# Optimization experiments

Hardware: AMD Instinct MI355X
Metric: run time of the kernel (lower is better)

Reference implementation:

```python
import jax, jax.numpy as jnp
import numpy as np

N, E, ESM, H, OUT, L, NG = 20000, 640000, 1280, 128, 256, 3, 64
NV, EV = 4, 1  # node/edge vector channels
MSG_S, MSG_V = 2 * H + H, 2 * NV + EV   # 384, 9
UPD_S, UPD_V = 2 * H, 2 * NV            # 256, 8


def _safe_norm(v):
    # exact ||v|| with zero (not nan) gradient at v == 0
    n2 = jnp.sum(v * v, axis=-1)
    pos = n2 > 0
    return jnp.sqrt(jnp.where(pos, n2, 1.0)) * pos


def _normalize(x, eps=1e-12):
    n = _safe_norm(x)[..., None]
    return jnp.where(n > 0, x / jnp.maximum(n, eps), 0.0)


def _ln(x, g, b, eps=1e-5):
    m = x.mean(-1, keepdims=True)
    v = ((x - m) ** 2).mean(-1, keepdims=True)
    return (x - m) / jnp.sqrt(v + eps) * g + b


def _gvp(s, v, Wss, Wvs, Wsv, Wvv, g, b):
    # s: [M, Cs], v: [M, Cv, 3]
    vn = _safe_norm(v)                                        # [M, Cv]
    s_out = jax.nn.gelu(_ln(s @ Wss.T + vn @ Wvs.T, g, b), approximate=False)
    v_out = jnp.einsum('mic,oi->moc', v, Wvv)                 # [M, Cvo, 3]
    v_out = v_out * jax.nn.sigmoid(s @ Wsv.T)[:, :, None]     # gate from input s
    return s_out, v_out


def _compute_node_vectors(coords, cb):
    ca_cb = _normalize(cb - coords)
    ca_next = jnp.roll(coords, -1, axis=0)
    d = (ca_next - coords).at[-1].set(0.0)
    d = _normalize(d)
    normal = _normalize(jnp.cross(ca_cb, d))
    t = (ca_next - jnp.roll(coords, 1, axis=0)).at[0].set(0.0).at[-1].set(0.0)
    t = _normalize(t)
    return jnp.stack([ca_cb, d, normal, t], axis=1)           # [N, 4, 3]


def setup_inputs() -> dict:
    key = jax.random.key(0)
    ks = jax.random.split(key, 32)

    def w(k, shape):
        return (jax.random.normal(k, shape, jnp.float32) / np.sqrt(shape[-1])).astype(jnp.float32)

    inp = {
        'esm_features': jax.random.normal(ks[0], (N, ESM), jnp.float32),
        'geometric_features': jax.random.normal(ks[1], (N, 15), jnp.float32),
        'node_coords': jax.random.normal(ks[2], (N, 3), jnp.float32) * 10.0,
        'edge_index': jax.random.randint(ks[3], (2, E), 0, N, jnp.int32),
        'edge_attr': jax.random.normal(ks[4], (E, 16), jnp.float32),
        'batch_index': jnp.sort(jax.random.randint(ks[5], (N,), 0, NG, jnp.int32)),
        # projections
        'node_proj_W': w(ks[6], (H, ESM + 9)), 'node_proj_b': jnp.zeros((H,), jnp.float32),
        'edge_proj_W': w(ks[7], (H, 13)), 'edge_proj_b': jnp.zeros((H,), jnp.float32),
        # message GVP (stacked over L layers)
        'msg_Wss': w(ks[8], (L, H, MSG_S)), 'msg_Wvs': w(ks[9], (L, H, MSG_V)),
        'msg_Wsv': w(ks[10], (L, NV, MSG_S)), 'msg_Wvv': w(ks[11], (L, NV, MSG_V)),
        'msg_ln_g': jnp.ones((L, H), jnp.float32), 'msg_ln_b': jnp.zeros((L, H), jnp.float32),
        # update GVP
        'upd_Wss': w(ks[12], (L, H, UPD_S)), 'upd_Wvs': w(ks[13], (L, H, UPD_V)),
        'upd_Wsv': w(ks[14], (L, NV, UPD_S)), 'upd_Wvv': w(ks[15], (L, NV, UPD_V)),
        'upd_ln_g': jnp.ones((L, H), jnp.float32), 'upd_ln_b': jnp.zeros((L, H), jnp.float32),
        # heads
        'node_out_W': w(ks[16], (ESM, H)), 'node_out_b': jnp.zeros((ESM,), jnp.float32),
        'graph_out_W': w(ks[17], (OUT, H)), 'graph_out_b': jnp.zeros((OUT,), jnp.float32),
    }
    return inp


def reference(esm_features, geometric_features, node_coords, edge_index, edge_attr,
              batch_index, node_proj_W, node_proj_b, edge_proj_W, edge_proj_b,
              msg_Wss, msg_Wvs, msg_Wsv, msg_Wvv, msg_ln_g, msg_ln_b,
              upd_Wss, upd_Wvs, upd_Wsv, upd_Wvv, upd_ln_g, upd_ln_b,
              node_out_W, node_out_b, graph_out_W, graph_out_b):
    n = esm_features.shape[0]
    cb = geometric_features[:, 3:6]
    geo_scalar = geometric_features[:, 6:15]
    node_s = jnp.concatenate([esm_features, geo_scalar], -1) @ node_proj_W.T + node_proj_b
    node_v = _compute_node_vectors(node_coords, cb)
    edge_s = jnp.concatenate([edge_attr[:, 0:2], edge_attr[:, 5:]], -1) @ edge_proj_W.T + edge_proj_b
    edge_v = edge_attr[:, 2:5][:, None, :]                    # [E, 1, 3]
    src, dst = edge_index[0], edge_index[1]
    for l in range(msg_Wss.shape[0]):
        ms = jnp.concatenate([node_s[src], node_s[dst], edge_s], -1)   # [E, 3H]
        mv = jnp.concatenate([node_v[src], node_v[dst], edge_v], 1)    # [E, 9, 3]
        ms, mv = _gvp(ms, mv, msg_Wss[l], msg_Wvs[l], msg_Wsv[l], msg_Wvv[l],
                      msg_ln_g[l], msg_ln_b[l])
        ag_s = jnp.zeros((n, ms.shape[1]), ms.dtype).at[dst].add(ms)
        ag_v = jnp.zeros((n, mv.shape[1], 3), mv.dtype).at[dst].add(mv)
        us = jnp.concatenate([node_s, ag_s], -1)
        uv = jnp.concatenate([node_v, ag_v], 1)
        ns, nv = _gvp(us, uv, upd_Wss[l], upd_Wvs[l], upd_Wsv[l], upd_Wvv[l],
                      upd_ln_g[l], upd_ln_b[l])
        node_s = node_s + ns
        node_v = node_v + nv
    updated_nodes = node_s @ node_out_W.T + node_out_b
    gfeat = node_s @ graph_out_W.T + graph_out_b
    cnt = jax.ops.segment_sum(jnp.ones((n,), gfeat.dtype), batch_index, NG)
    graph_emb = jax.ops.segment_sum(gfeat, batch_index, NG) / jnp.maximum(cnt, 1.0)[:, None]
    return graph_emb, updated_nodes
```

## Files before the change

### kernel.cpp

```cpp
#include <hip/hip_runtime.h>
#include <math.h>

#define DEVI __device__ __forceinline__

namespace {

constexpr int NN = 20000;
constexpr int NE = 640000;

typedef __attribute__((ext_vector_type(8))) short s8v;
typedef __attribute__((ext_vector_type(4))) float f4v;

DEVI float gelu_f(float x){ return 0.5f*x*(1.0f+erff(x*0.70710678118654752440f)); }
DEVI float gelu_t(float x){
  float u = x*x;
  float z = x*(1.59576912f + 0.07135481f*u);
  return x / (1.f + __expf(-z));
}
DEVI float sigm(float x){ return 1.0f/(1.0f+expf(-x)); }
DEVI float sigm_f(float x){ return 1.0f/(1.0f+__expf(-x)); }
DEVI unsigned bf_rne(float f){ unsigned u=__float_as_uint(f); return (u + 0x7fffu + ((u>>16)&1u)) >> 16; }

struct F3{ float x,y,z; };
DEVI F3 sub3(F3 a, F3 b){ return F3{a.x-b.x, a.y-b.y, a.z-b.z}; }
DEVI F3 cross3(F3 a, F3 b){ return F3{a.y*b.z-a.z*b.y, a.z*b.x-a.x*b.z, a.x*b.y-a.y*b.x}; }
DEVI F3 snorm3(F3 v){
  float n2 = v.x*v.x+v.y*v.y+v.z*v.z;
  if(n2 > 0.f){ float inv = 1.0f/sqrtf(n2); return F3{v.x*inv, v.y*inv, v.z*inv}; }
  return F3{0.f,0.f,0.f};
}

__global__ void k_prep(const float* __restrict__ npW, const float* __restrict__ noW,
                       const float* __restrict__ goW,
                       const float* __restrict__ mWss, const float* __restrict__ mWvs,
                       const float* __restrict__ uWss, const float* __restrict__ uWvs,
                       unsigned short* __restrict__ npW_bf, float* __restrict__ Wt_no,
                       float* __restrict__ Wt_go,
                       float* __restrict__ Wt_mss, float* __restrict__ Wt_mvs,
                       float* __restrict__ Wt_uss, float* __restrict__ Wt_uvs){
  int b = blockIdx.x, t = threadIdx.x;
  if(b >= 1563){
    int idx = (b-1563)*256 + t;
    if(idx < 128*1408){
      int r = idx/1408, c = idx-r*1408;
      npW_bf[idx] = (c<1289) ? (unsigned short)bf_rne(npW[(size_t)r*1289+c]) : (unsigned short)0;
    }
    return;
  }
  const float* src; float* dst; int R,C,ld,base,elems;
  if(b<640){ src=noW; dst=Wt_no; R=1280;C=128;ld=128; base=0; elems=163840; }
  else if(b<768){ src=goW; dst=Wt_go; R=256;C=128;ld=128; base=640; elems=32768; }
  else {
    int bb=b-768; int l=bb/265; int r=bb-l*265;
    if(r<128){ src=mWss+(size_t)l*128*384; dst=Wt_mss+(size_t)l*256*128; R=128;C=256;ld=384; base=768+l*265; elems=32768; }
    else if(r<133){ src=mWvs+(size_t)l*128*9; dst=Wt_mvs+(size_t)l*9*128; R=128;C=9;ld=9; base=768+l*265+128; elems=1152; }
    else if(r<261){ src=uWss+(size_t)l*128*256; dst=Wt_uss+(size_t)l*256*128; R=128;C=256;ld=256; base=768+l*265+133; elems=32768; }
    else { src=uWvs+(size_t)l*128*8; dst=Wt_uvs+(size_t)l*8*128; R=128;C=8;ld=8; base=768+l*265+261; elems=1024; }
  }
  int idx=(b-base)*256+t;
  if(idx>=elems) return;
  int r=idx/C, c=idx%C;
  dst[c*R+r] = src[r*ld+c];
}

__global__ void k_conv(const float* __restrict__ esm, const float* __restrict__ geo,
                       unsigned short* __restrict__ esm_bf){
  int idx = blockIdx.x*256 + threadIdx.x;
  if(idx >= 20000*176) return;
  int r = idx/176, c = idx - r*176;
  int k = c*8;
  float v0,v1,v2,v3,v4,v5,v6,v7;
  if(k+8 <= 1280){
    const float4* p = reinterpret_cast<const float4*>(esm + (size_t)r*1280 + k);
    float4 x=p[0], y=p[1];
    v0=x.x;v1=x.y;v2=x.z;v3=x.w;v4=y.x;v5=y.y;v6=y.z;v7=y.w;
  } else {
    float vv[8];
#pragma unroll
    for(int j=0;j<8;j++){
      int kk=k+j;
      vv[j] = (kk<1280)? esm[(size_t)r*1280+kk] : ((kk<1289)? geo[r*15+6+(kk-1280)] : 0.f);
    }
    v0=vv[0];v1=vv[1];v2=vv[2];v3=vv[3];v4=vv[4];v5=vv[5];v6=vv[6];v7=vv[7];
  }
  uint4 w;
  w.x = bf_rne(v0) | (bf_rne(v1)<<16);
  w.y = bf_rne(v2) | (bf_rne(v3)<<16);
  w.z = bf_rne(v4) | (bf_rne(v5)<<16);
  w.w = bf_rne(v6) | (bf_rne(v7)<<16);
  reinterpret_cast<uint4*>(esm_bf)[idx] = w;
}

__global__ __launch_bounds__(256,4) void k_init(
    const unsigned short* __restrict__ esm_bf, const unsigned short* __restrict__ npW_bf,
    float* __restrict__ part){
  int t = threadIdx.x;
  int b = blockIdx.x;
  int ks = b & 3, nb = b >> 2;
  int wv = t>>6, lane = t&63;
  int row0 = nb*64 + wv*16;
  int arow = row0 + (lane&15);
  int arc = (arow < NN) ? arow : (NN-1);
  int kb = (lane>>4)*8;
  const unsigned short* ap = esm_bf + (size_t)arc*1408 + ks*352 + kb;
  const unsigned short* bp = npW_bf + (size_t)(lane&15)*1408 + ks*352 + kb;
// ... 15 lines not shown
    int o = nt*16+col;
#pragma unroll
    for(int r=0;r<4;r++){
      int row = row0 + r4 + r;
      if(row<NN) po[(size_t)row*128+o] = acc[nt][r];
    }
  }
}

__global__ void k_reduce(const float* __restrict__ part, const float* __restrict__ bias,
                         float* __restrict__ node_s){
  int idx = blockIdx.x*256 + threadIdx.x;
  int o = idx & 127;
  node_s[idx] = bias[o] + part[idx] + part[(size_t)NN*128+idx]
              + part[2*(size_t)NN*128+idx] + part[3*(size_t)NN*128+idx];
}

__global__ void k_nodevec(const float* __restrict__ coords, const float* __restrict__ geo,
                          float* __restrict__ node_v,
                          int* __restrict__ counts, int* __restrict__ cntg){
  int n = blockIdx.x*256 + threadIdx.x;
  if(n<64) cntg[n]=0;
  if(n>=NN) return;
  counts[n]=0;
  F3 c  {coords[n*3], coords[n*3+1], coords[n*3+2]};
  F3 cb {geo[n*15+3], geo[n*15+4], geo[n*15+5]};
  F3 cacb = snorm3(sub3(cb, c));
  F3 d{0.f,0.f,0.f};
  if(n < NN-1){
    F3 nx {coords[(n+1)*3], coords[(n+1)*3+1], coords[(n+1)*3+2]};
    d = snorm3(sub3(nx, c));
  }
  F3 nor = snorm3(cross3(cacb, d));
  F3 tv{0.f,0.f,0.f};
  if(n>0 && n<NN-1){
    F3 nx {coords[(n+1)*3], coords[(n+1)*3+1], coords[(n+1)*3+2]};
    F3 pv {coords[(n-1)*3], coords[(n-1)*3+1], coords[(n-1)*3+2]};
    tv = snorm3(sub3(nx, pv));
  }
  float* p = node_v + n*12;
  p[0]=cacb.x; p[1]=cacb.y; p[2]=cacb.z;
  p[3]=d.x;    p[4]=d.y;    p[5]=d.z;
  p[6]=nor.x;  p[7]=nor.y;  p[8]=nor.z;
  p[9]=tv.x;   p[10]=tv.y;  p[11]=tv.z;
}

__global__ void k_hist(const int* __restrict__ eidx, const int* __restrict__ batch,
                       int* __restrict__ counts, int* __restrict__ cntg){
  int i = blockIdx.x*256+threadIdx.x;
  if(i<NE) atomicAdd(&counts[eidx[NE+i]], 1);
  if(i<NN) atomicAdd(&cntg[batch[i]], 1);
}
__global__ void k_scan1(const int* __restrict__ counts, int* __restrict__ bsums){
  __shared__ int red[256];
  int b=blockIdx.x, t=threadIdx.x;
  int base=b*512;
  int v=0;
  for(int i=t;i<512;i+=256){ int g=base+i; if(g<NN) v+=counts[g]; }
  red[t]=v; __syncthreads();
// ... 88 lines not shown
#pragma unroll
    for(int n=0;n<16;n++){
      float4 s4 = *reinterpret_cast<const float4*>(&s_l[n][k]);
      acc[n] = fmaf(s4.x,w0,acc[n]); acc[n] = fmaf(s4.y,w1,acc[n]);
      acc[n] = fmaf(s4.z,w2,acc[n]); acc[n] = fmaf(s4.w,w3,acc[n]);
    }
  }
  const float* Wv = Wt_vs + h*4*128;
#pragma unroll
  for(int j=0;j<4;j++){
    float w = Wv[j*128+o];
#pragma unroll
    for(int n=0;n<16;n++) acc[n] += nv_l[n][j]*w;
  }
  float* P = h ? P_b : P_a;
#pragma unroll
  for(int n=0;n<16;n++) P[(size_t)(n0+n)*128+o] = acc[n];
}

__global__ void k_econst3(const float* __restrict__ mWss, const float* __restrict__ mWvs,
                          const float* __restrict__ mWsv, const float* __restrict__ mWvv,
                          const float* __restrict__ Wep, const float* __restrict__ epb,
                          float* __restrict__ econ){
  int l = blockIdx.x;
  const float* Wss = mWss + (size_t)l*128*384;
  const float* Wvs = mWvs + (size_t)l*128*9;
  const float* Wsv = mWsv + (size_t)l*4*384;
  const float* Wvv = mWvv + (size_t)l*4*9;
  float* ec = econ + (size_t)l*2048;
  int t=threadIdx.x;
  for(int idx=t; idx<13*128; idx+=256){
    int j=idx>>7, o=idx&127;
    float s=0.f;
    for(int k=0;k<128;k++) s += Wss[o*384+256+k]*Wep[k*13+j];
    ec[j*128+o]=s;
  }
  for(int o=t;o<128;o+=256){
    float s=0.f;
    for(int k=0;k<128;k++) s += Wss[o*384+256+k]*epb[k];
    ec[1664+o]=s;
    ec[1792+o]=Wvs[o*9+8];
  }
  if(t<52){ int c=t/13,j=t%13; float s=0.f; for(int k=0;k<128;k++) s+=Wsv[c*384+256+k]*Wep[k*13+j]; ec[1920+t]=s; }
  if(t<4){ float s=0.f; for(int k=0;k<128;k++) s+=Wsv[t*384+256+k]*epb[k]; ec[1972+t]=s; ec[1976+t]=Wvv[t*9+8]; }
}

__global__ __launch_bounds__(256,4) void k_edge(
    const float* __restrict__ ea_s, const float* __restrict__ ec,
    unsigned* __restrict__ preS2, float* __restrict__ preG){
  int t = threadIdx.x;
  int lane = t&63;
  int wid = blockIdx.x*4 + (t>>6);
  float mex[13], mey[13];
#pragma unroll
  for(int j=0;j<13;j++){ mex[j]=ec[j*128+lane]; mey[j]=ec[j*128+64+lane]; }
  float bx=ec[1664+lane], by=ec[1664+64+lane];
  float w8x=ec[1792+lane], w8y=ec[1792+64+lane];
  int cg = (lane<4)?lane:0;
  float grc[13];
// ... 34 lines not shown
      g=fmaf(grc[3],e3,g);  g=fmaf(grc[4],e4,g);  g=fmaf(grc[5],e5,g);
      g=fmaf(grc[6],e6,g);  g=fmaf(grc[7],e7,g);  g=fmaf(grc[8],e8,g);
      g=fmaf(grc[9],e9,g);  g=fmaf(grc[10],e10,g); g=fmaf(grc[11],e11,g);
      g=fmaf(grc[12],e12,g);
      preG[(size_t)e*8+lane] = g;
    } else if(lane<7){
      float evv = (lane==4)?evx:((lane==5)?evy:evz);
      preG[(size_t)e*8+lane] = evv;
    }
  }
}

#define DECLST(P) unsigned P##w=0; float P##pax=0.f,P##pay=0.f,P##g8=0.f,P##ev=0.f,P##ga=0.f,P##va=0.f;
#define LOADST(P, IDX) do{ int _p=(IDX); int _s=srcp[_p]; \
  P##w   = preS2[_p*64 + lane]; \
  P##pax = P_a[_s*128+lane]; P##pay = P_a[_s*128+64+lane]; \
  if(lane<12){ P##g8 = preG[_p*8+cv]; P##ev = preG[_p*8+4+xv]; \
               P##ga = G_a[_s*4+cv];  P##va = V_a[_s*12+lane]; } \
}while(0)
#define COMPUTE(P) do{ \
  float px = __uint_as_float(P##w<<16); \
  float py = __uint_as_float(P##w & 0xffff0000u); \
  float pre0 = px + P##pax + PBx; \
  float pre1 = py + P##pay + PBy; \
  float sm = pre0+pre1; \
  float sq = pre0*pre0 + pre1*pre1; \
  _Pragma("unroll") \
  for(int m=32;m;m>>=1){ sm += __shfl_xor(sm,m); sq += __shfl_xor(sq,m); } \
  float mean = sm*0.0078125f; \
  float var  = fmaf(sq,0.0078125f, -mean*mean); \
  float rstd = rsqrtf((var>0.f?var:0.f) + 1e-5f); \
// ... 6 lines not shown
  } \
}while(0)

__global__ __launch_bounds__(256,8) void k_msg(
                      const float* __restrict__ P_a, const float* __restrict__ P_b,
                      const float* __restrict__ G_a, const float* __restrict__ G_b,
                      const float* __restrict__ V_a, const float* __restrict__ V_b,
                      const unsigned* __restrict__ preS2, const float* __restrict__ preG,
                      const int* __restrict__ srcp, const int* __restrict__ offs,
                      const float* __restrict__ ec,
                      const float* __restrict__ lng, const float* __restrict__ lnb,
                      float* __restrict__ ag_s, float* __restrict__ ag_v){
  int t = threadIdx.x;
  int n = blockIdx.x*4 + (t>>6);
  int lane = t&63;
  float PBx = P_b[n*128+lane], PBy = P_b[n*128+64+lane];
  float LGx = lng[lane], LGy = lng[64+lane];
  float LBx = lnb[lane], LBy = lnb[64+lane];
  int cv = lane/3, xv = lane - cv*3;
  float vbk=0.f, gbn=0.f, wvc=0.f;
  if(lane<12){
    vbk = V_b[n*12+lane];
    gbn = G_b[n*4+cv];
    wvc = ec[1976+cv];
  }
  float accx=0.f, accy=0.f, avk=0.f;
  int beg = offs[n], end = offs[n+1];
  DECLST(a_) DECLST(b_)
  int idx = beg;
  if(beg < end) LOADST(a_, beg);
  while(idx + 1 < end){
    LOADST(b_, idx+1);
    COMPUTE(a_);
    if(idx + 2 < end) LOADST(a_, idx+2);
    COMPUTE(b_);
    idx += 2;
  }
  if(idx < end) COMPUTE(a_);
  ag_s[n*128+lane]    = accx;
  ag_s[n*128+64+lane] = accy;
  if(lane<12) ag_v[n*12+lane] = avk;
}

__global__ __launch_bounds__(256,4) void k_update(
                         float* __restrict__ node_s, float* __restrict__ node_v,
                         const float* __restrict__ ag_s, const float* __restrict__ ag_v,
                         const float* __restrict__ Wt_ss, const float* __restrict__ Wt_vs,
                         const float* __restrict__ Wsv, const float* __restrict__ Wvv,
                         const float* __restrict__ lng, const float* __restrict__ lnb){
  __shared__ float us[16][260];
  __shared__ float pre[16][129];
  __shared__ float uv[16][24];
  __shared__ float uvn[16][8];
  __shared__ float stats[16][2];
  __shared__ float gate_l[16][4];
  int t = threadIdx.x;
  int n0 = blockIdx.x*16;
  for(int idx=t; idx<2048; idx+=256){
    int n = idx>>7, k = idx&127;
    us[n][k]     = node_s[(size_t)(n0+n)*128+k];
    us[n][128+k] = ag_s[(size_t)(n0+n)*128+k];
  }
  for(int idx=t; idx<384; idx+=256){
    int n = idx/24, k = idx%24;
    uv[n][k] = (k<12) ? node_v[(n0+n)*12+k] : ag_v[(n0+n)*12 + (k-12)];
  }
  __syncthreads();
  if(t<128){
    int n=t>>3, j=t&7;
    float x=uv[n][j*3], y=uv[n][j*3+1], z=uv[n][j*3+2];
    float n2=x*x+y*y+z*z;
    uvn[n][j] = n2>0.f ? sqrtf(n2) : 0.f;
  }
  __syncthreads();
  int o = t&127, h = t>>7;
  float acc[8];
#pragma unroll
  for(int i=0;i<8;i++) acc[i]=0.f;
  for(int k=0;k<256;k+=4){
    float w0=Wt_ss[(k+0)*128+o], w1=Wt_ss[(k+1)*128+o], w2=Wt_ss[(k+2)*128+o], w3=Wt_ss[(k+3)*128+o];
#pragma unroll
    for(int i=0;i<8;i++){
      float4 s4 = *reinterpret_cast<const float4*>(&us[h*8+i][k]);
      acc[i] = fmaf(s4.x,w0,acc[i]); acc[i] = fmaf(s4.y,w1,acc[i]);
      acc[i] = fmaf(s4.z,w2,acc[i]); acc[i] = fmaf(s4.w,w3,acc[i]);
    }
  }
#pragma unroll
  for(int j=0;j<8;j++){
    float w = Wt_vs[j*128+o];
#pragma unroll
    for(int i=0;i<8;i++) acc[i] += uvn[h*8+i][j]*w;
  }
#pragma unroll
  for(int i=0;i<8;i++) pre[h*8+i][o] = acc[i];
  __syncthreads();
  {
    int n = t>>4, p = t&15;
    float s=0.f;
#pragma unroll
    for(int q=0;q<8;q++) s += pre[n][p*8+q];
#pragma unroll
    for(int m=8;m;m>>=1) s += __shfl_xor(s,m);
    float mean = s*(1.f/128.f);
    float v=0.f;
#pragma unroll
    for(int q=0;q<8;q++){ float d=pre[n][p*8+q]-mean; v += d*d; }
#pragma unroll
    for(int m=8;m;m>>=1) v += __shfl_xor(v,m);
    if(p==0){ stats[n][0]=mean; stats[n][1]=rsqrtf(v*(1.f/128.f)+1e-5f); }
  }
  __syncthreads();
  {
    float LG = lng[o], LB = lnb[o];
#pragma unroll
    for(int i=0;i<8;i++){
      int n = h*8+i;
      float hh = (pre[n][o]-stats[n][0])*stats[n][1]*LG + LB;
      node_s[(size_t)(n0+n)*128+o] += gelu_f(hh);
    }
  }
  {
    int n = t>>4, c = t&3, p = (t>>2)&3;
    float g=0.f;
    int kb = p*64;
    for(int k=0;k<64;k+=4){
      float4 s4 = *reinterpret_cast<const float4*>(&us[n][kb+k]);
      g = fmaf(s4.x,Wsv[c*256+kb+k],g);   g = fmaf(s4.y,Wsv[c*256+kb+k+1],g);
      g = fmaf(s4.z,Wsv[c*256+kb+k+2],g); g = fmaf(s4.w,Wsv[c*256+kb+k+3],g);
    }
    g += __shfl_xor(g,4);
    g += __shfl_xor(g,8);
    if(p==0) gate_l[n][c] = sigm(g);
  }
  __syncthreads();
  if(t<192){
    int n = t/12, k = t%12, c = k/3, x = k-c*3;
    float s=0.f;
#pragma unroll
    for(int j=0;j<8;j++) s += Wvv[c*8+j]*uv[n][j*3+x];
    node_v[(n0+n)*12+k] += s*gate_l[n][c];
  }
}

__global__ __launch_bounds__(256,8) void k_out(
    const float* __restrict__ node_s, const float* __restrict__ Wt_no,
    const float* __restrict__ nob, float* __restrict__ out){
  __shared__ float s_l[32][132];
  int t = threadIdx.x;
  int n0 = blockIdx.x*32;
  int oc0 = blockIdx.y*256;
  {
    const float4* g = reinterpret_cast<const float4*>(node_s + (size_t)n0*128);
    for(int i=t;i<1024;i+=256){
      int n=i>>5, kq=i&31;
      *reinterpret_cast<float4*>(&s_l[n][kq*4]) = g[i];
    }
  }
  __syncthreads();
  int oq = t&63, ng = t>>6;
  int o = oc0 + oq*4;
  float4 acc[8];
#pragma unroll
  for(int i=0;i<8;i++) acc[i]=float4{0.f,0.f,0.f,0.f};
  for(int k=0;k<128;k+=4){
    float4 w0 = *reinterpret_cast<const float4*>(&Wt_no[(k+0)*1280+o]);
    float4 w1 = *reinterpret_cast<const float4*>(&Wt_no[(k+1)*1280+o]);
    float4 w2 = *reinterpret_cast<const float4*>(&Wt_no[(k+2)*1280+o]);
    float4 w3 = *reinterpret_cast<const float4*>(&Wt_no[(k+3)*1280+o]);
#pragma unroll
    for(int i=0;i<8;i++){
      float4 s = *reinterpret_cast<const float4*>(&s_l[ng*8+i][k]);
      acc[i].x=fmaf(s.x,w0.x,acc[i].x); acc[i].y=fmaf(s.x,w0.y,acc[i].y);
      acc[i].z=fmaf(s.x,w0.z,acc[i].z); acc[i].w=fmaf(s.x,w0.w,acc[i].w);
      acc[i].x=fmaf(s.y,w1.x,acc[i].x); acc[i].y=fmaf(s.y,w1.y,acc[i].y);
      acc[i].z=fmaf(s.y,w1.z,acc[i].z); acc[i].w=fmaf(s.y,w1.w,acc[i].w);
      acc[i].x=fmaf(s.z,w2.x,acc[i].x); acc[i].y=fmaf(s.z,w2.y,acc[i].y);
      acc[i].z=fmaf(s.z,w2.z,acc[i].z); acc[i].w=fmaf(s.z,w2.w,acc[i].w);
      acc[i].x=fmaf(s.w,w3.x,acc[i].x); acc[i].y=fmaf(s.w,w3.y,acc[i].y);
      acc[i].z=fmaf(s.w,w3.z,acc[i].z); acc[i].w=fmaf(s.w,w3.w,acc[i].w);
    }
  }
  float4 b4 = *reinterpret_cast<const float4*>(&nob[o]);
#pragma unroll
  for(int i=0;i<8;i++){
    int row = n0 + ng*8 + i;
    float4 r{acc[i].x+b4.x, acc[i].y+b4.y, acc[i].z+b4.z, acc[i].w+b4.w};
    *reinterpret_cast<float4*>(&out[16384 + (size_t)row*1280 + o]) = r;
  }
}

__global__ __launch_bounds__(256,4) void k_gfeat(
                        const float* __restrict__ node_s, const float* __restrict__ Wt,
                        const int* __restrict__ batch, float* __restrict__ gacc){
  __shared__ float s_l[16][128];
  __shared__ int b_l[16];
  int t=threadIdx.x, n0=blockIdx.x*16;
  for(int idx=t; idx<2048; idx+=256){ int n=idx>>7,k=idx&127; s_l[n][k]=node_s[(size_t)(n0+n)*128+k]; }
  if(t<16) b_l[t]=batch[n0+t];
  __syncthreads();
  int o=t;
  float acc[16];
#pragma unroll
  for(int i=0;i<16;i++) acc[i]=0.f;
  for(int k=0;k<128;k+=4){
    float w0=Wt[(k+0)*256+o], w1=Wt[(k+1)*256+o], w2=Wt[(k+2)*256+o], w3=Wt[(k+3)*256+o];
#pragma unroll
    for(int n=0;n<16;n++){
      float4 s4 = *reinterpret_cast<const float4*>(&s_l[n][k]);
      acc[n] = fmaf(s4.x,w0,acc[n]); acc[n] = fmaf(s4.y,w1,acc[n]);
      acc[n] = fmaf(s4.z,w2,acc[n]); acc[n] = fmaf(s4.w,w3,acc[n]);
    }
  }
  float run=0.f; int cur=b_l[0];
#pragma unroll
  for(int n=0;n<16;n++){
    int g=b_l[n];
    if(g!=cur){ atomicAdd(&gacc[cur*256+o], run); run=0.f; cur=g; }
    run += acc[n];
  }
  atomicAdd(&gacc[cur*256+o], run);
}

__global__ void k_gfin(const float* __restrict__ gacc, const int* __restrict__ cntg,
                       const float* __restrict__ gob, float* __restrict__ out){
  int g=blockIdx.x, o=threadIdx.x;
  int c=cntg[g];
  out[g*256+o] = (c>0) ? (gacc[g*256+o]/(float)c + gob[o]) : 0.f;
}

}

extern "C" void kernel_launch(void* const* d_in, const int* in_sizes, int n_in,
                              void* d_out, int out_size, void* d_ws, size_t ws_size,
                              hipStream_t stream){
  (void)in_sizes; (void)n_in; (void)out_size;
// ... 54 lines not shown
  float* gacc   = (float*)ALLOC((size_t)64*256*4);
  int* counts = (int*)ALLOC((size_t)NN*4);
  int* offs   = (int*)ALLOC((size_t)(NN+1)*4);
  int* cursor = (int*)ALLOC((size_t)NN*4);
  int* bsums  = (int*)ALLOC((size_t)64*4);
  int* cntg   = (int*)ALLOC((size_t)64*4);
  int* srcp   = (int*)ALLOC((size_t)NE*4);
  float* ea_s = (float*)ALLOC((size_t)NE*16*4);
  unsigned* preS2 = (unsigned*)ALLOC((size_t)NE*64*4);
  float* preG     = (float*)ALLOC((size_t)NE*8*4);
  if(off > ws_size) return;
  float* part = (float*)preS2;

  hipMemsetAsync(gacc, 0, (size_t)64*256*4, stream);

  k_prep<<<2267,256,0,stream>>>(npW, noW, goW, mWss, mWvs, uWss, uWvs,
                                npW_bf, Wt_no, Wt_go, Wt_mss, Wt_mvs, Wt_uss, Wt_uvs);
  k_conv<<<13750,256,0,stream>>>(esm, geo, esm_bf);
  k_init<<<1252,256,0,stream>>>(esm_bf, npW_bf, part);
  k_reduce<<<10000,256,0,stream>>>(part, npb, node_s);
  k_nodevec<<<79,256,0,stream>>>(coords, geo, node_v, counts, cntg);
  k_hist<<<2500,256,0,stream>>>(eidx, batch, counts, cntg);
  k_scan1<<<40,256,0,stream>>>(counts, bsums);
  k_scan23<<<40,256,0,stream>>>(counts, bsums, offs, cursor);
  k_fill<<<2500,256,0,stream>>>(eidx, cursor, eattr, srcp, ea_s);
  k_econst3<<<3,256,0,stream>>>(mWss, mWvs, mWsv, mWvv, epW, epb, econ);

  for(int l=0;l<3;l++){
    k_pre<<<1250,256,0,stream>>>(node_s, node_v,
                                 Wt_mss + (size_t)l*256*128, Wt_mvs + (size_t)l*9*128,
                                 mWsv + (size_t)l*4*384, mWvv + (size_t)l*4*9,
                                 P_a, P_b, G_a, G_b, V_a, V_b);
    k_edge<<<20000,256,0,stream>>>(ea_s, econ + (size_t)l*2048, preS2, preG);
    k_msg<<<5000,256,0,stream>>>(P_a, P_b, G_a, G_b, V_a, V_b, preS2, preG, srcp, offs,
                                 econ + (size_t)l*2048, mlg + (size_t)l*128, mlb + (size_t)l*128,
                                 ag_s, ag_v);
    k_update<<<1250,256,0,stream>>>(node_s, node_v, ag_s, ag_v,
                                    Wt_uss + (size_t)l*256*128, Wt_uvs + (size_t)l*8*128,
                                    uWsv + (size_t)l*4*256, uWvv + (size_t)l*4*8,
                                    ulg + (size_t)l*128, ulb + (size_t)l*128);
  }
  k_out<<<dim3(625,5),256,0,stream>>>(node_s, Wt_no, nob, out);
  k_gfeat<<<1250,256,0,stream>>>(node_s, Wt_go, batch, gacc);
  k_gfin<<<64,256,0,stream>>>(gacc, cntg, gob, out);
}
```

Measured before the change: 1.549 ms.

## Fuse prep kernels, fold next-layer pre into update, merge output kernels

Merges the weight-transpose, bf16 conversion, node-vector and edge-constant kernels into one large k_prep launch. The next layer's message precompute (P/G/V projections) is folded into the update kernel, so updated node features are reused from shared memory instead of being reloaded. The output and graph-feature GEMMs are combined into one launch. P_a/P_b are stored interleaved so k_msg can read them with float2 loads. This cuts launch count and global round-trips, at the cost of a longer update kernel with more barriers and shared-memory state.

New measurement: 1.572 ms. No clear change (+1.5%).

```diff
diff --git a/kernel.cpp b/kernel.cpp
--- a/kernel.cpp
+++ b/kernel.cpp
@@ -33,13 +33,36 @@
 __global__ void k_prep(const float* __restrict__ npW, const float* __restrict__ noW,
                        const float* __restrict__ goW,
                        const float* __restrict__ mWss, const float* __restrict__ mWvs,
+                       const float* __restrict__ mWsv, const float* __restrict__ mWvv,
                        const float* __restrict__ uWss, const float* __restrict__ uWvs,
-                       unsigned short* __restrict__ npW_bf, float* __restrict__ Wt_no,
-                       float* __restrict__ Wt_go,
+                       const float* __restrict__ Wep, const float* __restrict__ epb,
+                       const float* __restrict__ esm, const float* __restrict__ geo,
+                       const float* __restrict__ coords,
+                       unsigned short* __restrict__ npW_bf, unsigned short* __restrict__ esm_bf,
+                       float* __restrict__ Wt_no, float* __restrict__ Wt_go,
                        float* __restrict__ Wt_mss, float* __restrict__ Wt_mvs,
-                       float* __restrict__ Wt_uss, float* __restrict__ Wt_uvs){
+                       float* __restrict__ Wt_uss, float* __restrict__ Wt_uvs,
+                       float* __restrict__ econ, float* __restrict__ node_v,
+                       int* __restrict__ counts, int* __restrict__ cntg){
   int b = blockIdx.x, t = threadIdx.x;
-  if(b >= 1563){
+  if(b < 1563){
+    const float* src; float* dst; int R,C,ld,base,elems;
+    if(b<640){ src=noW; dst=Wt_no; R=1280;C=128;ld=128; base=0; elems=163840; }
+    else if(b<768){ src=goW; dst=Wt_go; R=256;C=128;ld=128; base=640; elems=32768; }
+    else {
+      int bb=b-768; int l=bb/265; int r=bb-l*265;
+      if(r<128){ src=mWss+(size_t)l*128*384; dst=Wt_mss+(size_t)l*256*128; R=128;C=256;ld=384; base=768+l*265; elems=32768; }
+      else if(r<133){ src=mWvs+(size_t)l*128*9; dst=Wt_mvs+(size_t)l*9*128; R=128;C=9;ld=9; base=768+l*265+128; elems=1152; }
+      else if(r<261){ src=uWss+(size_t)l*128*256; dst=Wt_uss+(size_t)l*256*128; R=128;C=256;ld=256; base=768+l*265+133; elems=32768; }
+      else { src=uWvs+(size_t)l*128*8; dst=Wt_uvs+(size_t)l*8*128; R=128;C=8;ld=8; base=768+l*265+261; elems=1024; }
+    }
+    int idx=(b-base)*256+t;
+    if(idx>=elems) return;
+    int r=idx/C, c=idx%C;
+    dst[c*R+r] = src[r*ld+c];
+    return;
+  }
+  if(b < 2267){
     int idx = (b-1563)*256 + t;
     if(idx < 128*1408){
       int r = idx/1408, c = idx-r*1408;
@@ -47,48 +70,82 @@
     }
     return;
   }
-  const float* src; float* dst; int R,C,ld,base,elems;
-  if(b<640){ src=noW; dst=Wt_no; R=1280;C=128;ld=128; base=0; elems=163840; }
-  else if(b<768){ src=goW; dst=Wt_go; R=256;C=128;ld=128; base=640; elems=32768; }
-  else {
-    int bb=b-768; int l=bb/265; int r=bb-l*265;
-    if(r<128){ src=mWss+(size_t)l*128*384; dst=Wt_mss+(size_t)l*256*128; R=128;C=256;ld=384; base=768+l*265; elems=32768; }
-    else if(r<133){ src=mWvs+(size_t)l*128*9; dst=Wt_mvs+(size_t)l*9*128; R=128;C=9;ld=9; base=768+l*265+128; elems=1152; }
-    else if(r<261){ src=uWss+(size_t)l*128*256; dst=Wt_uss+(size_t)l*256*128; R=128;C=256;ld=256; base=768+l*265+133; elems=32768; }
-    else { src=uWvs+(size_t)l*128*8; dst=Wt_uvs+(size_t)l*8*128; R=128;C=8;ld=8; base=768+l*265+261; elems=1024; }
-  }
-  int idx=(b-base)*256+t;
-  if(idx>=elems) return;
-  int r=idx/C, c=idx%C;
-  dst[c*R+r] = src[r*ld+c];
-}
-
-__global__ void k_conv(const float* __restrict__ esm, const float* __restrict__ geo,
-                       unsigned short* __restrict__ esm_bf){
-  int idx = blockIdx.x*256 + threadIdx.x;
-  if(idx >= 20000*176) return;
-  int r = idx/176, c = idx - r*176;
-  int k = c*8;
-  float v0,v1,v2,v3,v4,v5,v6,v7;
-  if(k+8 <= 1280){
-    const float4* p = reinterpret_cast<const float4*>(esm + (size_t)r*1280 + k);
-    float4 x=p[0], y=p[1];
-    v0=x.x;v1=x.y;v2=x.z;v3=x.w;v4=y.x;v5=y.y;v6=y.z;v7=y.w;
-  } else {
-    float vv[8];
-#pragma unroll
-    for(int j=0;j<8;j++){
-      int kk=k+j;
-      vv[j] = (kk<1280)? esm[(size_t)r*1280+kk] : ((kk<1289)? geo[r*15+6+(kk-1280)] : 0.f);
-    }
-    v0=vv[0];v1=vv[1];v2=vv[2];v3=vv[3];v4=vv[4];v5=vv[5];v6=vv[6];v7=vv[7];
-  }
-  uint4 w;
-  w.x = bf_rne(v0) | (bf_rne(v1)<<16);
-  w.y = bf_rne(v2) | (bf_rne(v3)<<16);
-  w.z = bf_rne(v4) | (bf_rne(v5)<<16);
-  w.w = bf_rne(v6) | (bf_rne(v7)<<16);
-  reinterpret_cast<uint4*>(esm_bf)[idx] = w;
+  if(b < 16017){
+    int idx = (b-2267)*256 + t;
+    if(idx >= 20000*176) return;
+    int r = idx/176, c = idx - r*176;
+    int k = c*8;
+    float v0,v1,v2,v3,v4,v5,v6,v7;
+    if(k+8 <= 1280){
+      const float4* p = reinterpret_cast<const float4*>(esm + (size_t)r*1280 + k);
+      float4 x=p[0], y=p[1];
+      v0=x.x;v1=x.y;v2=x.z;v3=x.w;v4=y.x;v5=y.y;v6=y.z;v7=y.w;
+    } else {
+      float vv[8];
+#pragma unroll
+      for(int j=0;j<8;j++){
+        int kk=k+j;
+        vv[j] = (kk<1280)? esm[(size_t)r*1280+kk] : ((kk<1289)? geo[r*15+6+(kk-1280)] : 0.f);
+      }
+      v0=vv[0];v1=vv[1];v2=vv[2];v3=vv[3];v4=vv[4];v5=vv[5];v6=vv[6];v7=vv[7];
+    }
+    uint4 w;
+    w.x = bf_rne(v0) | (bf_rne(v1)<<16);
+    w.y = bf_rne(v2) | (bf_rne(v3)<<16);
+    w.z = bf_rne(v4) | (bf_rne(v5)<<16);
+    w.w = bf_rne(v6) | (bf_rne(v7)<<16);
+    reinterpret_cast<uint4*>(esm_bf)[idx] = w;
+    return;
+  }
+  if(b < 16096){
+    int n = (b-16017)*256 + t;
+    if(n<64) cntg[n]=0;
+    if(n>=NN) return;
+    counts[n]=0;
+    F3 c  {coords[n*3], coords[n*3+1], coords[n*3+2]};
+    F3 cb {geo[n*15+3], geo[n*15+4], geo[n*15+5]};
+    F3 cacb = snorm3(sub3(cb, c));
+    F3 d{0.f,0.f,0.f};
+    if(n < NN-1){
+      F3 nx {coords[(n+1)*3], coords[(n+1)*3+1], coords[(n+1)*3+2]};
+      d = snorm3(sub3(nx, c));
+    }
+    F3 nor = snorm3(cross3(cacb, d));
+    F3 tv{0.f,0.f,0.f};
+    if(n>0 && n<NN-1){
+      F3 nx {coords[(n+1)*3], coords[(n+1)*3+1], coords[(n+1)*3+2]};
+      F3 pv {coords[(n-1)*3], coords[(n-1)*3+1], coords[(n-1)*3+2]};
+      tv = snorm3(sub3(nx, pv));
+    }
+    float* p = node_v + n*12;
+    p[0]=cacb.x; p[1]=cacb.y; p[2]=cacb.z;
+    p[3]=d.x;    p[4]=d.y;    p[5]=d.z;
+    p[6]=nor.x;  p[7]=nor.y;  p[8]=nor.z;
+    p[9]=tv.x;   p[10]=tv.y;  p[11]=tv.z;
+    return;
+  }
+  {
+    int l = b - 16096;
+    const float* Wss = mWss + (size_t)l*128*384;
+    const float* Wvs = mWvs + (size_t)l*128*9;
+    const float* Wsv = mWsv + (size_t)l*4*384;
+    const float* Wvv = mWvv + (size_t)l*4*9;
+    float* ec = econ + (size_t)l*2048;
+    for(int idx=t; idx<13*128; idx+=256){
+      int j=idx>>7, o=idx&127;
+      float s=0.f;
+      for(int k=0;k<128;k++) s += Wss[o*384+256+k]*Wep[k*13+j];
+      ec[j*128+o]=s;
+    }
+    for(int o=t;o<128;o+=256){
+      float s=0.f;
+      for(int k=0;k<128;k++) s += Wss[o*384+256+k]*epb[k];
+      ec[1664+o]=s;
+      ec[1792+o]=Wvs[o*9+8];
+    }
+    if(t<52){ int c=t/13,j=t%13; float s=0.f; for(int k=0;k<128;k++) s+=Wsv[c*384+256+k]*Wep[k*13+j]; ec[1920+t]=s; }
+    if(t<4){ float s=0.f; for(int k=0;k<128;k++) s+=Wsv[t*384+256+k]*epb[k]; ec[1972+t]=s; ec[1976+t]=Wvv[t*9+8]; }
+  }
 }
 
 __global__ __launch_bounds__(256,4) void k_init(
@@ -134,35 +191,6 @@
   int o = idx & 127;
   node_s[idx] = bias[o] + part[idx] + part[(size_t)NN*128+idx]
               + part[2*(size_t)NN*128+idx] + part[3*(size_t)NN*128+idx];
-}
-
-__global__ void k_nodevec(const float* __restrict__ coords, const float* __restrict__ geo,
-                          float* __restrict__ node_v,
-                          int* __restrict__ counts, int* __restrict__ cntg){
-  int n = blockIdx.x*256 + threadIdx.x;
-  if(n<64) cntg[n]=0;
-  if(n>=NN) return;
-  counts[n]=0;
-  F3 c  {coords[n*3], coords[n*3+1], coords[n*3+2]};
-  F3 cb {geo[n*15+3], geo[n*15+4], geo[n*15+5]};
-  F3 cacb = snorm3(sub3(cb, c));
-  F3 d{0.f,0.f,0.f};
-  if(n < NN-1){
-    F3 nx {coords[(n+1)*3], coords[(n+1)*3+1], coords[(n+1)*3+2]};
-    d = snorm3(sub3(nx, c));
-  }
-  F3 nor = snorm3(cross3(cacb, d));
-  F3 tv{0.f,0.f,0.f};
-  if(n>0 && n<NN-1){
-    F3 nx {coords[(n+1)*3], coords[(n+1)*3+1], coords[(n+1)*3+2]};
-    F3 pv {coords[(n-1)*3], coords[(n-1)*3+1], coords[(n-1)*3+2]};
-    tv = snorm3(sub3(nx, pv));
-  }
-  float* p = node_v + n*12;
-  p[0]=cacb.x; p[1]=cacb.y; p[2]=cacb.z;
-  p[3]=d.x;    p[4]=d.y;    p[5]=d.z;
-  p[6]=nor.x;  p[7]=nor.y;  p[8]=nor.z;
-  p[9]=tv.x;   p[10]=tv.y;  p[11]=tv.z;
 }
 
 __global__ void k_hist(const int* __restrict__ eidx, const int* __restrict__ batch,
@@ -281,35 +309,9 @@
     for(int n=0;n<16;n++) acc[n] += nv_l[n][j]*w;
   }
   float* P = h ? P_b : P_a;
-#pragma unroll
-  for(int n=0;n<16;n++) P[(size_t)(n0+n)*128+o] = acc[n];
-}
-
-__global__ void k_econst3(const float* __restrict__ mWss, const float* __restrict__ mWvs,
-                          const float* __restrict__ mWsv, const float* __restrict__ mWvv,
-                          const float* __restrict__ Wep, const float* __restrict__ epb,
-                          float* __restrict__ econ){
-  int l = blockIdx.x;
-  const float* Wss = mWss + (size_t)l*128*384;
-  const float* Wvs = mWvs + (size_t)l*128*9;
-  const float* Wsv = mWsv + (size_t)l*4*384;
-  const float* Wvv = mWvv + (size_t)l*4*9;
-  float* ec = econ + (size_t)l*2048;
-  int t=threadIdx.x;
-  for(int idx=t; idx<13*128; idx+=256){
-    int j=idx>>7, o=idx&127;
-    float s=0.f;
-    for(int k=0;k<128;k++) s += Wss[o*384+256+k]*Wep[k*13+j];
-    ec[j*128+o]=s;
-  }
-  for(int o=t;o<128;o+=256){
-    float s=0.f;
-    for(int k=0;k<128;k++) s += Wss[o*384+256+k]*epb[k];
-    ec[1664+o]=s;
-    ec[1792+o]=Wvs[o*9+8];
-  }
-  if(t<52){ int c=t/13,j=t%13; float s=0.f; for(int k=0;k<128;k++) s+=Wsv[c*384+256+k]*Wep[k*13+j]; ec[1920+t]=s; }
-  if(t<4){ float s=0.f; for(int k=0;k<128;k++) s+=Wsv[t*384+256+k]*epb[k]; ec[1972+t]=s; ec[1976+t]=Wvv[t*9+8]; }
+  int oo = ((o&63)<<1) | (o>>6);
+#pragma unroll
+  for(int n=0;n<16;n++) P[(size_t)(n0+n)*128+oo] = acc[n];
 }
 
 __global__ __launch_bounds__(256,4) void k_edge(
@@ -374,7 +376,8 @@
 #define DECLST(P) unsigned P##w=0; float P##pax=0.f,P##pay=0.f,P##g8=0.f,P##ev=0.f,P##ga=0.f,P##va=0.f;
 #define LOADST(P, IDX) do{ int _p=(IDX); int _s=srcp[_p]; \
   P##w   = preS2[_p*64 + lane]; \
-  P##pax = P_a[_s*128+lane]; P##pay = P_a[_s*128+64+lane]; \
+  float2 _pa = *reinterpret_cast<const float2*>(P_a + _s*128 + 2*lane); \
+  P##pax = _pa.x; P##pay = _pa.y; \
   if(lane<12){ P##g8 = preG[_p*8+cv]; P##ev = preG[_p*8+4+xv]; \
                P##ga = G_a[_s*4+cv];  P##va = V_a[_s*12+lane]; } \
 }while(0)
@@ -411,7 +414,8 @@
   int t = threadIdx.x;
   int n = blockIdx.x*4 + (t>>6);
   int lane = t&63;
-  float PBx = P_b[n*128+lane], PBy = P_b[n*128+64+lane];
+  float2 pb2 = *reinterpret_cast<const float2*>(P_b + n*128 + 2*lane);
+  float PBx = pb2.x, PBy = pb2.y;
   float LGx = lng[lane], LGy = lng[64+lane];
   float LBx = lnb[lane], LBy = lnb[64+lane];
   int cv = lane/3, xv = lane - cv*3;
@@ -439,18 +443,25 @@
   if(lane<12) ag_v[n*12+lane] = avk;
 }
 
-__global__ __launch_bounds__(256,4) void k_update(
+__global__ __launch_bounds__(256,4) void k_updpre(
                          float* __restrict__ node_s, float* __restrict__ node_v,
                          const float* __restrict__ ag_s, const float* __restrict__ ag_v,
                          const float* __restrict__ Wt_ss, const float* __restrict__ Wt_vs,
                          const float* __restrict__ Wsv, const float* __restrict__ Wvv,
-                         const float* __restrict__ lng, const float* __restrict__ lnb){
+                         const float* __restrict__ lng, const float* __restrict__ lnb,
+                         int has_pre,
+                         const float* __restrict__ nWt_ss, const float* __restrict__ nWt_vs,
+                         const float* __restrict__ nWsv, const float* __restrict__ nWvv,
+                         float* __restrict__ P_a, float* __restrict__ P_b,
+                         float* __restrict__ G_a, float* __restrict__ G_b,
+                         float* __restrict__ V_a, float* __restrict__ V_b){
   __shared__ float us[16][260];
   __shared__ float pre[16][129];
   __shared__ float uv[16][24];
   __shared__ float uvn[16][8];
   __shared__ float stats[16][2];
   __shared__ float gate_l[16][4];
+  __shared__ float nvp[16][4];
   int t = threadIdx.x;
   int n0 = blockIdx.x*16;
   for(int idx=t; idx<2048; idx+=256){
@@ -468,54 +479,6 @@
     float x=uv[n][j*3], y=uv[n][j*3+1], z=uv[n][j*3+2];
     float n2=x*x+y*y+z*z;
     uvn[n][j] = n2>0.f ? sqrtf(n2) : 0.f;
-  }
-  __syncthreads();
-  int o = t&127, h = t>>7;
-  float acc[8];
-#pragma unroll
-  for(int i=0;i<8;i++) acc[i]=0.f;
-  for(int k=0;k<256;k+=4){
-    float w0=Wt_ss[(k+0)*128+o], w1=Wt_ss[(k+1)*128+o], w2=Wt_ss[(k+2)*128+o], w3=Wt_ss[(k+3)*128+o];
-#pragma unroll
-    for(int i=0;i<8;i++){
-      float4 s4 = *reinterpret_cast<const float4*>(&us[h*8+i][k]);
-      acc[i] = fmaf(s4.x,w0,acc[i]); acc[i] = fmaf(s4.y,w1,acc[i]);
-      acc[i] = fmaf(s4.z,w2,acc[i]); acc[i] = fmaf(s4.w,w3,acc[i]);
-    }
-  }
-#pragma unroll
-  for(int j=0;j<8;j++){
-    float w = Wt_vs[j*128+o];
-#pragma unroll
-    for(int i=0;i<8;i++) acc[i] += uvn[h*8+i][j]*w;
-  }
-#pragma unroll
-  for(int i=0;i<8;i++) pre[h*8+i][o] = acc[i];
-  __syncthreads();
-  {
-    int n = t>>4, p = t&15;
-    float s=0.f;
-#pragma unroll
-    for(int q=0;q<8;q++) s += pre[n][p*8+q];
-#pragma unroll
-    for(int m=8;m;m>>=1) s += __shfl_xor(s,m);
-    float mean = s*(1.f/128.f);
-    float v=0.f;
-#pragma unroll
-    for(int q=0;q<8;q++){ float d=pre[n][p*8+q]-mean; v += d*d; }
-#pragma unroll
-    for(int m=8;m;m>>=1) v += __shfl_xor(v,m);
-    if(p==0){ stats[n][0]=mean; stats[n][1]=rsqrtf(v*(1.f/128.f)+1e-5f); }
-  }
-  __syncthreads();
-  {
-    float LG = lng[o], LB = lnb[o];
-#pragma unroll
-    for(int i=0;i<8;i++){
-      int n = h*8+i;
-      float hh = (pre[n][o]-stats[n][0])*stats[n][1]*LG + LB;
-      node_s[(size_t)(n0+n)*128+o] += gelu_f(hh);
-    }
   }
   {
     int n = t>>4, c = t&3, p = (t>>2)&3;
@@ -531,92 +494,211 @@
     if(p==0) gate_l[n][c] = sigm(g);
   }
   __syncthreads();
+  int o = t&127, h = t>>7;
+  {
+    float acc[8];
+#pragma unroll
+    for(int i=0;i<8;i++) acc[i]=0.f;
+    for(int k=0;k<256;k+=4){
+      float w0=Wt_ss[(k+0)*128+o], w1=Wt_ss[(k+1)*128+o], w2=Wt_ss[(k+2)*128+o], w3=Wt_ss[(k+3)*128+o];
+#pragma unroll
+      for(int i=0;i<8;i++){
+        float4 s4 = *reinterpret_cast<const float4*>(&us[h*8+i][k]);
+        acc[i] = fmaf(s4.x,w0,acc[i]); acc[i] = fmaf(s4.y,w1,acc[i]);
+        acc[i] = fmaf(s4.z,w2,acc[i]); acc[i] = fmaf(s4.w,w3,acc[i]);
+      }
+    }
+#pragma unroll
+    for(int j=0;j<8;j++){
+      float w = Wt_vs[j*128+o];
+#pragma unroll
+      for(int i=0;i<8;i++) acc[i] += uvn[h*8+i][j]*w;
+    }
+#pragma unroll
+    for(int i=0;i<8;i++) pre[h*8+i][o] = acc[i];
+  }
+  __syncthreads();
+  {
+    int n = t>>4, p = t&15;
+    float s=0.f;
+#pragma unroll
+    for(int q=0;q<8;q++) s += pre[n][p*8+q];
+#pragma unroll
+    for(int m=8;m;m>>=1) s += __shfl_xor(s,m);
+    float mean = s*(1.f/128.f);
+    float v=0.f;
+#pragma unroll
+    for(int q=0;q<8;q++){ float d=pre[n][p*8+q]-mean; v += d*d; }
+#pragma unroll
+    for(int m=8;m;m>>=1) v += __shfl_xor(v,m);
+    if(p==0){ stats[n][0]=mean; stats[n][1]=rsqrtf(v*(1.f/128.f)+1e-5f); }
+  }
+  __syncthreads();
+  {
+    float LG = lng[o], LB = lnb[o];
+#pragma unroll
+    for(int i=0;i<8;i++){
+      int n = h*8+i;
+      float hh = (pre[n][o]-stats[n][0])*stats[n][1]*LG + LB;
+      float val = us[n][o] + gelu_f(hh);
+      node_s[(size_t)(n0+n)*128+o] = val;
+      us[n][o] = val;
+    }
+  }
+  float nvv = 0.f; int vn=0, vk=0;
   if(t<192){
-    int n = t/12, k = t%12, c = k/3, x = k-c*3;
+    vn = t/12; vk = t%12;
+    int c = vk/3, x = vk-c*3;
     float s=0.f;
 #pragma unroll
-    for(int j=0;j<8;j++) s += Wvv[c*8+j]*uv[n][j*3+x];
-    node_v[(n0+n)*12+k] += s*gate_l[n][c];
-  }
-}
-
-__global__ __launch_bounds__(256,8) void k_out(
+    for(int j=0;j<8;j++) s += Wvv[c*8+j]*uv[vn][j*3+x];
+    nvv = uv[vn][vk] + s*gate_l[vn][c];
+  }
+  __syncthreads();
+  if(t<192){
+    uv[vn][vk] = nvv;
+    node_v[(n0+vn)*12+vk] = nvv;
+  }
+  if(!has_pre) return;
+  __syncthreads();
+  if(t<64){
+    int n=t>>2, j=t&3;
+    float x=uv[n][j*3], y=uv[n][j*3+1], z=uv[n][j*3+2];
+    float n2=x*x+y*y+z*z;
+    nvp[n][j] = n2>0.f ? sqrtf(n2) : 0.f;
+  }
+  if(t<192){
+    int n=t/12, k=t%12, c=k/3, x=k-c*3;
+    float va=0.f, vb=0.f;
+#pragma unroll
+    for(int j=0;j<4;j++){
+      float vv = uv[n][j*3+x];
+      va += nWvv[c*9+j]*vv;
+      vb += nWvv[c*9+4+j]*vv;
+    }
+    V_a[(n0+n)*12+k]=va; V_b[(n0+n)*12+k]=vb;
+  }
+  if(t<128){
+    int n=t>>3, c=(t>>1)&3, hh=t&1;
+    const float* w = nWsv + c*384 + hh*128;
+    float g=0.f;
+    for(int k=0;k<128;k+=4){
+      float4 s4 = *reinterpret_cast<const float4*>(&us[n][k]);
+      g = fmaf(s4.x,w[k],g); g = fmaf(s4.y,w[k+1],g);
+      g = fmaf(s4.z,w[k+2],g); g = fmaf(s4.w,w[k+3],g);
+    }
+    (hh ? G_b : G_a)[(n0+n)*4+c] = g;
+  }
+  __syncthreads();
+  {
+    float acc[16];
+#pragma unroll
+    for(int i=0;i<16;i++) acc[i]=0.f;
+    const float* Wb = nWt_ss + h*128*128;
+    for(int k=0;k<128;k+=4){
+      float w0=Wb[(k+0)*128+o], w1=Wb[(k+1)*128+o], w2=Wb[(k+2)*128+o], w3=Wb[(k+3)*128+o];
+#pragma unroll
+      for(int n=0;n<16;n++){
+        float4 s4 = *reinterpret_cast<const float4*>(&us[n][k]);
+        acc[n] = fmaf(s4.x,w0,acc[n]); acc[n] = fmaf(s4.y,w1,acc[n]);
+        acc[n] = fmaf(s4.z,w2,acc[n]); acc[n] = fmaf(s4.w,w3,acc[n]);
+      }
+    }
+    const float* Wv = nWt_vs + h*4*128;
+#pragma unroll
+    for(int j=0;j<4;j++){
+      float w = Wv[j*128+o];
+#pragma unroll
+      for(int n=0;n<16;n++) acc[n] += nvp[n][j]*w;
+    }
+    float* P = h ? P_b : P_a;
+    int oo = ((o&63)<<1) | (o>>6);
+#pragma unroll
+    for(int n=0;n<16;n++) P[(size_t)(n0+n)*128+oo] = acc[n];
+  }
+}
+
+__global__ __launch_bounds__(256,8) void k_outg(
     const float* __restrict__ node_s, const float* __restrict__ Wt_no,
-    const float* __restrict__ nob, float* __restrict__ out){
-  __shared__ float s_l[32][132];
+    const float* __restrict__ nob, const float* __restrict__ Wt_go,
+    const int* __restrict__ batch, float* __restrict__ gacc,
+    float* __restrict__ out){
+  __shared__ float sbuf[32*132];
+  __shared__ int b_l[16];
   int t = threadIdx.x;
-  int n0 = blockIdx.x*32;
-  int oc0 = blockIdx.y*256;
-  {
-    const float4* g = reinterpret_cast<const float4*>(node_s + (size_t)n0*128);
-    for(int i=t;i<1024;i+=256){
-      int n=i>>5, kq=i&31;
-      *reinterpret_cast<float4*>(&s_l[n][kq*4]) = g[i];
-    }
-  }
-  __syncthreads();
-  int oq = t&63, ng = t>>6;
-  int o = oc0 + oq*4;
-  float4 acc[8];
-#pragma unroll
-  for(int i=0;i<8;i++) acc[i]=float4{0.f,0.f,0.f,0.f};
-  for(int k=0;k<128;k+=4){
-    float4 w0 = *reinterpret_cast<const float4*>(&Wt_no[(k+0)*1280+o]);
-    float4 w1 = *reinterpret_cast<const float4*>(&Wt_no[(k+1)*1280+o]);
-    float4 w2 = *reinterpret_cast<const float4*>(&Wt_no[(k+2)*1280+o]);
-    float4 w3 = *reinterpret_cast<const float4*>(&Wt_no[(k+3)*1280+o]);
+  int b = blockIdx.x;
+  if(b < 3125){
+    int nb = b % 625, yc = b / 625;
+    int n0 = nb*32;
+    int oc0 = yc*256;
+    {
+      const float4* g = reinterpret_cast<const float4*>(node_s + (size_t)n0*128);
+      for(int i=t;i<1024;i+=256){
+        int n=i>>5, kq=i&31;
+        *reinterpret_cast<float4*>(&sbuf[n*132 + kq*4]) = g[i];
+      }
+    }
+    __syncthreads();
+    int oq = t&63, ng = t>>6;
+    int o = oc0 + oq*4;
+    float4 acc[8];
+#pragma unroll
+    for(int i=0;i<8;i++) acc[i]=float4{0.f,0.f,0.f,0.f};
+    for(int k=0;k<128;k+=4){
+      float4 w0 = *reinterpret_cast<const float4*>(&Wt_no[(k+0)*1280+o]);
+      float4 w1 = *reinterpret_cast<const float4*>(&Wt_no[(k+1)*1280+o]);
+      float4 w2 = *reinterpret_cast<const float4*>(&Wt_no[(k+2)*1280+o]);
+      float4 w3 = *reinterpret_cast<const float4*>(&Wt_no[(k+3)*1280+o]);
+#pragma unroll
+      for(int i=0;i<8;i++){
+        float4 s = *reinterpret_cast<const float4*>(&sbuf[(ng*8+i)*132 + k]);
+        acc[i].x=fmaf(s.x,w0.x,acc[i].x); acc[i].y=fmaf(s.x,w0.y,acc[i].y);
+        acc[i].z=fmaf(s.x,w0.z,acc[i].z); acc[i].w=fmaf(s.x,w0.w,acc[i].w);
+        acc[i].x=fmaf(s.y,w1.x,acc[i].x); acc[i].y=fmaf(s.y,w1.y,acc[i].y);
+        acc[i].z=fmaf(s.y,w1.z,acc[i].z); acc[i].w=fmaf(s.y,w1.w,acc[i].w);
+        acc[i].x=fmaf(s.z,w2.x,acc[i].x); acc[i].y=fmaf(s.z,w2.y,acc[i].y);
+        acc[i].z=fmaf(s.z,w2.z,acc[i].z); acc[i].w=fmaf(s.z,w2.w,acc[i].w);
+        acc[i].x=fmaf(s.w,w3.x,acc[i].x); acc[i].y=fmaf(s.w,w3.y,acc[i].y);
+        acc[i].z=fmaf(s.w,w3.z,acc[i].z); acc[i].w=fmaf(s.w,w3.w,acc[i].w);
+      }
+    }
+    float4 b4 = *reinterpret_cast<const float4*>(&nob[o]);
 #pragma unroll
     for(int i=0;i<8;i++){
-      float4 s = *reinterpret_cast<const float4*>(&s_l[ng*8+i][k]);
-      acc[i].x=fmaf(s.x,w0.x,acc[i].x); acc[i].y=fmaf(s.x,w0.y,acc[i].y);
-      acc[i].z=fmaf(s.x,w0.z,acc[i].z); acc[i].w=fmaf(s.x,w0.w,acc[i].w);
-      acc[i].x=fmaf(s.y,w1.x,acc[i].x); acc[i].y=fmaf(s.y,w1.y,acc[i].y);
-      acc[i].z=fmaf(s.y,w1.z,acc[i].z); acc[i].w=fmaf(s.y,w1.w,acc[i].w);
-      acc[i].x=fmaf(s.z,w2.x,acc[i].x); acc[i].y=fmaf(s.z,w2.y,acc[i].y);
-      acc[i].z=fmaf(s.z,w2.z,acc[i].z); acc[i].w=fmaf(s.z,w2.w,acc[i].w);
-      acc[i].x=fmaf(s.w,w3.x,acc[i].x); acc[i].y=fmaf(s.w,w3.y,acc[i].y);
-      acc[i].z=fmaf(s.w,w3.z,acc[i].z); acc[i].w=fmaf(s.w,w3.w,acc[i].w);
-    }
-  }
-  float4 b4 = *reinterpret_cast<const float4*>(&nob[o]);
-#pragma unroll
-  for(int i=0;i<8;i++){
-    int row = n0 + ng*8 + i;
-    float4 r{acc[i].x+b4.x, acc[i].y+b4.y, acc[i].z+b4.z, acc[i].w+b4.w};
-    *reinterpret_cast<float4*>(&out[16384 + (size_t)row*1280 + o]) = r;
-  }
-}
-
-__global__ __launch_bounds__(256,4) void k_gfeat(
-                        const float* __restrict__ node_s, const float* __restrict__ Wt,
-                        const int* __restrict__ batch, float* __restrict__ gacc){
-  __shared__ float s_l[16][128];
-  __shared__ int b_l[16];
-  int t=threadIdx.x, n0=blockIdx.x*16;
-  for(int idx=t; idx<2048; idx+=256){ int n=idx>>7,k=idx&127; s_l[n][k]=node_s[(size_t)(n0+n)*128+k]; }
-  if(t<16) b_l[t]=batch[n0+t];
-  __syncthreads();
-  int o=t;
-  float acc[16];
-#pragma unroll
-  for(int i=0;i<16;i++) acc[i]=0.f;
-  for(int k=0;k<128;k+=4){
-    float w0=Wt[(k+0)*256+o], w1=Wt[(k+1)*256+o], w2=Wt[(k+2)*256+o], w3=Wt[(k+3)*256+o];
+      int row = n0 + ng*8 + i;
+      float4 r{acc[i].x+b4.x, acc[i].y+b4.y, acc[i].z+b4.z, acc[i].w+b4.w};
+      *reinterpret_cast<float4*>(&out[16384 + (size_t)row*1280 + o]) = r;
+    }
+  } else {
+    int n0 = (b-3125)*16;
+    for(int idx=t; idx<2048; idx+=256){
+      int n=idx>>7, k=idx&127;
+      sbuf[n*128+k] = node_s[(size_t)(n0+n)*128+k];
+    }
+    if(t<16) b_l[t]=batch[n0+t];
+    __syncthreads();
+    int o=t;
+    float acc[16];
+#pragma unroll
+    for(int i=0;i<16;i++) acc[i]=0.f;
+    for(int k=0;k<128;k+=4){
+      float w0=Wt_go[(k+0)*256+o], w1=Wt_go[(k+1)*256+o], w2=Wt_go[(k+2)*256+o], w3=Wt_go[(k+3)*256+o];
+#pragma unroll
+      for(int n=0;n<16;n++){
+        float4 s4 = *reinterpret_cast<const float4*>(&sbuf[n*128+k]);
+        acc[n] = fmaf(s4.x,w0,acc[n]); acc[n] = fmaf(s4.y,w1,acc[n]);
+        acc[n] = fmaf(s4.z,w2,acc[n]); acc[n] = fmaf(s4.w,w3,acc[n]);
+      }
+    }
+    float run=0.f; int cur=b_l[0];
 #pragma unroll
     for(int n=0;n<16;n++){
-      float4 s4 = *reinterpret_cast<const float4*>(&s_l[n][k]);
-      acc[n] = fmaf(s4.x,w0,acc[n]); acc[n] = fmaf(s4.y,w1,acc[n]);
-      acc[n] = fmaf(s4.z,w2,acc[n]); acc[n] = fmaf(s4.w,w3,acc[n]);
-    }
-  }
-  float run=0.f; int cur=b_l[0];
-#pragma unroll
-  for(int n=0;n<16;n++){
-    int g=b_l[n];
-    if(g!=cur){ atomicAdd(&gacc[cur*256+o], run); run=0.f; cur=g; }
-    run += acc[n];
-  }
-  atomicAdd(&gacc[cur*256+o], run);
+      int g=b_l[n];
+      if(g!=cur){ atomicAdd(&gacc[cur*256+o], run); run=0.f; cur=g; }
+      run += acc[n];
+    }
+    atomicAdd(&gacc[cur*256+o], run);
+  }
 }
 
 __global__ void k_gfin(const float* __restrict__ gacc, const int* __restrict__ cntg,
@@ -701,33 +783,35 @@
 
   hipMemsetAsync(gacc, 0, (size_t)64*256*4, stream);
 
-  k_prep<<<2267,256,0,stream>>>(npW, noW, goW, mWss, mWvs, uWss, uWvs,
-                                npW_bf, Wt_no, Wt_go, Wt_mss, Wt_mvs, Wt_uss, Wt_uvs);
-  k_conv<<<13750,256,0,stream>>>(esm, geo, esm_bf);
+  k_prep<<<16099,256,0,stream>>>(npW, noW, goW, mWss, mWvs, mWsv, mWvv, uWss, uWvs,
+                                 epW, epb, esm, geo, coords,
+                                 npW_bf, esm_bf, Wt_no, Wt_go, Wt_mss, Wt_mvs,
+                                 Wt_uss, Wt_uvs, econ, node_v, counts, cntg);
   k_init<<<1252,256,0,stream>>>(esm_bf, npW_bf, part);
   k_reduce<<<10000,256,0,stream>>>(part, npb, node_s);
-  k_nodevec<<<79,256,0,stream>>>(coords, geo, node_v, counts, cntg);
   k_hist<<<2500,256,0,stream>>>(eidx, batch, counts, cntg);
   k_scan1<<<40,256,0,stream>>>(counts, bsums);
   k_scan23<<<40,256,0,stream>>>(counts, bsums, offs, cursor);
   k_fill<<<2500,256,0,stream>>>(eidx, cursor, eattr, srcp, ea_s);
-  k_econst3<<<3,256,0,stream>>>(mWss, mWvs, mWsv, mWvv, epW, epb, econ);
-
+
+  k_pre<<<1250,256,0,stream>>>(node_s, node_v,
+                               Wt_mss, Wt_mvs, mWsv, mWvv,
+                               P_a, P_b, G_a, G_b, V_a, V_b);
   for(int l=0;l<3;l++){
-    k_pre<<<1250,256,0,stream>>>(node_s, node_v,
-                                 Wt_mss + (size_t)l*256*128, Wt_mvs + (size_t)l*9*128,
-                                 mWsv + (size_t)l*4*384, mWvv + (size_t)l*4*9,
-                                 P_a, P_b, G_a, G_b, V_a, V_b);
+    int ln = (l<2) ? (l+1) : l;
     k_edge<<<20000,256,0,stream>>>(ea_s, econ + (size_t)l*2048, preS2, preG);
     k_msg<<<5000,256,0,stream>>>(P_a, P_b, G_a, G_b, V_a, V_b, preS2, preG, srcp, offs,
                                  econ + (size_t)l*2048, mlg + (size_t)l*128, mlb + (size_t)l*128,
                                  ag_s, ag_v);
-    k_update<<<1250,256,0,stream>>>(node_s, node_v, ag_s, ag_v,
+    k_updpre<<<1250,256,0,stream>>>(node_s, node_v, ag_s, ag_v,
                                     Wt_uss + (size_t)l*256*128, Wt_uvs + (size_t)l*8*128,
                                     uWsv + (size_t)l*4*256, uWvv + (size_t)l*4*8,
-                                    ulg + (size_t)l*128, ulb + (size_t)l*128);
-  }
-  k_out<<<dim3(625,5),256,0,stream>>>(node_s, Wt_no, nob, out);
-  k_gfeat<<<1250,256,0,stream>>>(node_s, Wt_go, batch, gacc);
+                                    ulg + (size_t)l*128, ulb + (size_t)l*128,
+                                    (l<2) ? 1 : 0,
+                                    Wt_mss + (size_t)ln*256*128, Wt_mvs + (size_t)ln*9*128,
+                                    mWsv + (size_t)ln*4*384, mWvv + (size_t)ln*4*9,
+                                    P_a, P_b, G_a, G_b, V_a, V_b);
+  }
+  k_outg<<<4375,256,0,stream>>>(node_s, Wt_no, nob, Wt_go, batch, gacc, out);
   k_gfin<<<64,256,0,stream>>>(gacc, cntg, gob, out);
 }
```
